# Kernel optimization log

Hardware: AMD Instinct MI355X
Metric: run time of the kernel (lower is better)

Reference implementation:

```python
import jax, jax.numpy as jnp
import numpy as np

N, D, H, G = 4096, 256, 4, 16
HEAD_DIM = D // H
LN_EPS = 1e-5
TEMP = 5.0


def setup_inputs() -> dict:
    key = jax.random.key(0)
    ks = jax.random.split(key, 12)
    s = 0.05  # weight init scale
    nrm = lambda k, shp: jax.random.normal(k, shp, jnp.float32) * s
    return {
        "x": jax.random.normal(ks[0], (N, D), jnp.float32),
        "Wq": nrm(ks[1], (D, D)), "bq": jnp.zeros((D,), jnp.float32),
        "Wk": nrm(ks[2], (D, D)), "bk": jnp.zeros((D,), jnp.float32),
        "Wv": nrm(ks[3], (D, D)), "bv": jnp.zeros((D,), jnp.float32),
        "Wv1": nrm(ks[4], (D, D // 2)), "bv1": jnp.zeros((D // 2,), jnp.float32),
        "Wv2": nrm(ks[5], (D // 2, 1)), "bv2": jnp.zeros((1,), jnp.float32),
        "Wc1": nrm(ks[6], (2 * D, D)), "bc1": jnp.zeros((D,), jnp.float32),
        "Wc2": nrm(ks[7], (D, 1)), "bc2": jnp.zeros((1,), jnp.float32),
        "gamma": jnp.ones((D,), jnp.float32),
        "beta": jnp.zeros((D,), jnp.float32),
        "batch": jnp.sort(jax.random.randint(ks[8], (N,), 0, G)),
    }


def reference(x, Wq, bq, Wk, bk, Wv, bv, Wv1, bv1, Wv2, bv2,
              Wc1, bc1, Wc2, bc2, gamma, beta, batch):
    n = x.shape[0]
    # multi-head projections -> [N, H, head_dim]
    Q = (x @ Wq + bq).reshape(n, H, HEAD_DIM)
    K = (x @ Wk + bk).reshape(n, H, HEAD_DIM)
    V = (x @ Wv + bv).reshape(n, H, HEAD_DIM)

    # dense scores [N, N, H], block-diagonal mask by graph membership
    scores = jnp.einsum('nhd,mhd->nmh', Q, K) / np.sqrt(HEAD_DIM).astype(np.float32)
    same_graph = (batch[:, None] == batch[None, :])  # [N, N]
    scores = jnp.where(same_graph[:, :, None], scores, -jnp.inf)
    probs = jax.nn.softmax(scores, axis=1)  # softmax over keys m (dim=1, as in torch)
    # dropout is identity in eval mode
    attended = jnp.einsum('nmh,mhd->nhd', probs, V).reshape(n, D)

    # vulnerability detector MLP: D -> D/2 -> 1, sigmoid
    vuln = jax.nn.sigmoid(jax.nn.relu(x @ Wv1 + bv1) @ Wv2 + bv2)[:, 0]

    # global max pool per graph, broadcast back to nodes
    graph_ctx = jax.ops.segment_max(x, batch, num_segments=G, indices_are_sorted=True)[batch]
    combined = jnp.concatenate([x, graph_ctx], axis=1)  # [N, 2D]
    ctx = jax.nn.sigmoid(jnp.tanh(combined @ Wc1 + bc1) @ Wc2 + bc2)[:, 0]

    mha_avg = probs.mean(axis=(1, 2))  # [N]
    w = 0.6 * vuln + 0.3 * ctx + 0.1 * mha_avg

    # per-graph segment softmax with temperature 5.0
    w5 = w * TEMP
    seg_max = jax.ops.segment_max(w5, batch, num_segments=G, indices_are_sorted=True)[batch]
    e = jnp.exp(w5 - seg_max)
    seg_sum = jax.ops.segment_sum(e, batch, num_segments=G, indices_are_sorted=True)[batch]
    att = e / seg_sum  # [N]

    out = attended * att[:, None] + x  # residual
    # LayerNorm over last dim
    mu = out.mean(axis=-1, keepdims=True)
    var = out.var(axis=-1, keepdims=True)
    out = (out - mu) * jax.lax.rsqrt(var + LN_EPS) * gamma + beta
    return out, att
```

## Files before the change

### kernel.cpp

```cpp
#include <hip/hip_runtime.h>
#include <math.h>

#define N_NODES 4096
#define DIM 256
#define NH 4
#define NG 16
#define LN_EPS 1e-5f
#define TEMP 5.0f
#define RSLACK 4160
#define PS_STRIDE 72
#define BS_STRIDE 264
#define QT_MAX 24
#define KC3 3
#define ATTN_BLOCKS (NG * QT_MAX * KC3)

typedef __attribute__((ext_vector_type(8))) short short8;
typedef __attribute__((ext_vector_type(4))) short short4_t;
typedef __attribute__((ext_vector_type(4))) float f32x4;

__device__ __forceinline__ unsigned short f2bf(float f) {
    unsigned u = __builtin_bit_cast(unsigned, f);
    u += 0x7FFFu + ((u >> 16) & 1u);
    return (unsigned short)(u >> 16);
}
__device__ __forceinline__ float bf2f(unsigned short u) {
    return __builtin_bit_cast(float, (unsigned)u << 16);
}
__device__ __forceinline__ float fsigmoid(float z) { return 1.f / (1.f + __expf(-z)); }
__device__ __forceinline__ float ftanh(float z) {
    float t = __expf(2.f * z);
    return (t - 1.f) / (t + 1.f);
}
__device__ __forceinline__ int seg_search(const int* __restrict__ batch, int g) {
    int lo = 0, hi = N_NODES;
    while (lo < hi) {
        int mid = (lo + hi) >> 1;
        if (batch[mid] < g) lo = mid + 1; else hi = mid;
    }
    return lo;
}

__device__ __forceinline__ short8 afrag_f32(const float* __restrict__ x, int row, int k0) {
    float4 a = *(const float4*)&x[(size_t)row * 256 + k0];
    float4 b = *(const float4*)&x[(size_t)row * 256 + k0 + 4];
    short8 r = {(short)f2bf(a.x), (short)f2bf(a.y), (short)f2bf(a.z), (short)f2bf(a.w),
                (short)f2bf(b.x), (short)f2bf(b.y), (short)f2bf(b.z), (short)f2bf(b.w)};
    return r;
}

__device__ __forceinline__ void ldsB(const float* __restrict__ W, int ws, int bn,
                                     unsigned short* __restrict__ Bs) {
    int c4 = (threadIdx.x & 15) * 4;
    int r0 = threadIdx.x >> 4;
    for (int p = 0; p < 16; ++p) {
        int k = p * 16 + r0;
        float4 wv = *(const float4*)&W[(size_t)k * ws + bn + c4];
        Bs[(c4 + 0) * BS_STRIDE + k] = f2bf(wv.x);
        Bs[(c4 + 1) * BS_STRIDE + k] = f2bf(wv.y);
        Bs[(c4 + 2) * BS_STRIDE + k] = f2bf(wv.z);
        Bs[(c4 + 3) * BS_STRIDE + k] = f2bf(wv.w);
    }
    __syncthreads();
}

__global__ __launch_bounds__(256) void k1_kernel(
    const float* __restrict__ x,
    const float* __restrict__ Wq, const float* __restrict__ bq,
    const float* __restrict__ Wk, const float* __restrict__ bk,
    const float* __restrict__ Wv, const float* __restrict__ bv,
    const float* __restrict__ Wv1, const float* __restrict__ bv1,
    const float* __restrict__ Wv2, const float* __restrict__ Wc1,
    const float* __restrict__ bc1, const int* __restrict__ batch,
    unsigned short* __restrict__ Qb, unsigned short* __restrict__ Kb,
    unsigned short* __restrict__ Vt, float* __restrict__ vacc2,
    float* __restrict__ Tpre, float* __restrict__ gcw, int* __restrict__ seg) {
    __shared__ __align__(16) char smem[64 * BS_STRIDE * 2];
    int id = blockIdx.x, tid = threadIdx.x;
    if (id < 16) {
        int g = id;
        int s = seg_search(batch, g), e = seg_search(batch, g + 1);
        float* red = (float*)smem;
        float* gl  = (float*)smem + 1024;
        int c4 = (tid & 63) * 4, way = tid >> 6;
        float4 mx = {-INFINITY, -INFINITY, -INFINITY, -INFINITY};
        for (int i = s + way; i < e; i += 4) {
            float4 v = *(const float4*)&x[(size_t)i * DIM + c4];
            mx.x = fmaxf(mx.x, v.x); mx.y = fmaxf(mx.y, v.y);
            mx.z = fmaxf(mx.z, v.z); mx.w = fmaxf(mx.w, v.w);
        }
        *(float4*)&red[way * 256 + c4] = mx;
        __syncthreads();
        if (way == 0) {
#pragma unroll
            for (int j = 0; j < 4; ++j) {
                float mm = fmaxf(fmaxf(red[c4 + j], red[256 + c4 + j]),
                                 fmaxf(red[512 + c4 + j], red[768 + c4 + j]));
                gl[c4 + j] = bf2f(f2bf(mm));
            }
        }
        __syncthreads();
        float a0 = 0.f, a1 = 0.f, a2 = 0.f, a3 = 0.f;
        for (int k = 0; k < 256; k += 4) {
            a0 += gl[k + 0] * Wc1[(size_t)(256 + k + 0) * 256 + tid];
            a1 += gl[k + 1] * Wc1[(size_t)(256 + k + 1) * 256 + tid];
            a2 += gl[k + 2] * Wc1[(size_t)(256 + k + 2) * 256 + tid];
            a3 += gl[k + 3] * Wc1[(size_t)(256 + k + 3) * 256 + tid];
        }
        gcw[g * 256 + tid] = (a0 + a1) + (a2 + a3);
        return;
    }
    if (id == 16) {
        if (tid <= NG) seg[tid] = seg_search(batch, tid);
        return;
    }
    int u = id - 17;
    unsigned short* Bs = (unsigned short*)smem;
    int w = tid >> 6, lane = tid & 63, m = lane & 15, quad = lane >> 4;
    if (u < 768) {
        int z = u >> 8, r = u & 255, bx = r & 63, by = r >> 6;
        const float* W = (z == 0) ? Wq : (z == 1) ? Wk : Wv;
        const float* bias = (z == 0) ? bq : (z == 1) ? bk : bv;
        ldsB(W, 256, by * 64, Bs);
        int rowA = bx * 64 + 16 * w + m;
        short8 a[8];
#pragma unroll
        for (int ks = 0; ks < 8; ++ks) a[ks] = afrag_f32(x, rowA, ks * 32 + quad * 8);
        int node0 = bx * 64 + 16 * w + quad * 4;
#pragma unroll
        for (int nt = 0; nt < 4; ++nt) {
            f32x4 acc = {0.f, 0.f, 0.f, 0.f};
#pragma unroll
            for (int ks = 0; ks < 8; ++ks) {
                short8 b = *(const short8*)&Bs[(nt * 16 + m) * BS_STRIDE + ks * 32 + quad * 8];
                acc = __builtin_amdgcn_mfma_f32_16x16x32_bf16(a[ks], b, acc, 0, 0, 0);
            }
            int col = by * 64 + nt * 16 + m;
            float bb = bias[col];
            if (z == 0) {
#pragma unroll
                for (int r2 = 0; r2 < 4; ++r2)
                    Qb[(size_t)(node0 + r2) * 256 + col] = f2bf((acc[r2] + bb) * 0.125f);
            } else if (z == 1) {
#pragma unroll
                for (int r2 = 0; r2 < 4; ++r2)
                    Kb[(size_t)(node0 + r2) * 256 + col] = f2bf(acc[r2] + bb);
            } else {
                short4_t pk = {(short)f2bf(acc[0] + bb), (short)f2bf(acc[1] + bb),
                               (short)f2bf(acc[2] + bb), (short)f2bf(acc[3] + bb)};
                *(short4_t*)&Vt[(size_t)col * RSLACK + node0] = pk;
            }
        }
    } else if (u < 896) {
        int r = u - 768, bx = r & 63, by = r >> 6;
        ldsB(Wv1, 128, by * 64, Bs);
        int rowA = bx * 64 + 16 * w + m;
        short8 a[8];
#pragma unroll
        for (int ks = 0; ks < 8; ++ks) a[ks] = afrag_f32(x, rowA, ks * 32 + quad * 8);
        int node0 = bx * 64 + 16 * w + quad * 4;
        float psum[4] = {0.f, 0.f, 0.f, 0.f};
#pragma unroll
        for (int nt = 0; nt < 4; ++nt) {
            f32x4 acc = {0.f, 0.f, 0.f, 0.f};
#pragma unroll
            for (int ks = 0; ks < 8; ++ks) {
                short8 b = *(const short8*)&Bs[(nt * 16 + m) * BS_STRIDE + ks * 32 + quad * 8];
                acc = __builtin_amdgcn_mfma_f32_16x16x32_bf16(a[ks], b, acc, 0, 0, 0);
            }
            int col = by * 64 + nt * 16 + m;
            float bb = bv1[col], wv = Wv2[col];
#pragma unroll
            for (int r2 = 0; r2 < 4; ++r2) psum[r2] += fmaxf(acc[r2] + bb, 0.f) * wv;
        }
#pragma unroll
        for (int r2 = 0; r2 < 4; ++r2) {
#pragma unroll
            for (int mm = 1; mm < 16; mm <<= 1) psum[r2] += __shfl_xor(psum[r2], mm);
            if (m == 0) vacc2[(size_t)(node0 + r2) * 2 + by] = psum[r2];
        }
    } else {
        int r = u - 896, bx = r & 63, by = r >> 6;
        ldsB(Wc1, 256, by * 64, Bs);
        int rowA = bx * 64 + 16 * w + m;
        short8 a[8];
#pragma unroll
        for (int ks = 0; ks < 8; ++ks) a[ks] = afrag_f32(x, rowA, ks * 32 + quad * 8);
        int node0 = bx * 64 + 16 * w + quad * 4;
#pragma unroll
        for (int nt = 0; nt < 4; ++nt) {
            f32x4 acc = {0.f, 0.f, 0.f, 0.f};
#pragma unroll
            for (int ks = 0; ks < 8; ++ks) {
                short8 b = *(const short8*)&Bs[(nt * 16 + m) * BS_STRIDE + ks * 32 + quad * 8];
                acc = __builtin_amdgcn_mfma_f32_16x16x32_bf16(a[ks], b, acc, 0, 0, 0);
            }
            int col = by * 64 + nt * 16 + m;
            float bb = bc1[col];
#pragma unroll
            for (int r2 = 0; r2 < 4; ++r2)
                Tpre[(size_t)(node0 + r2) * 256 + col] = acc[r2] + bb;
        }
    }
}

__global__ __launch_bounds__(256) void k2_kernel(
    const float* __restrict__ Tpre, const float* __restrict__ gcw,
    const float* __restrict__ Wc2, const int* __restrict__ batch,
    const unsigned short* __restrict__ Qb, const unsigned short* __restrict__ Kb,
    const unsigned short* __restrict__ Vt, const int* __restrict__ seg,
    unsigned short* __restrict__ Opart, float* __restrict__ Lpart,
    float* __restrict__ cacc) {
    __shared__ __align__(16) unsigned short Ps[4 * 16 * PS_STRIDE];
    int tid = threadIdx.x;
    if (blockIdx.x < 256) {
        int nl = tid >> 4, cs = (tid & 15) * 16;
        int node = blockIdx.x * 16 + nl;
        int g = batch[node];
        float sum = 0.f;
#pragma unroll
        for (int j = 0; j < 16; ++j) {
            int c = cs + j;
            sum += ftanh(Tpre[(size_t)node * 256 + c] + gcw[g * 256 + c]) * Wc2[c];
        }
#pragma unroll
        for (int mm = 1; mm < 16; mm <<= 1) sum += __shfl_xor(sum, mm);
        if ((tid & 15) == 0) cacc[node] = sum;
        return;
    }
    int w = tid >> 6, lane = tid & 63, m = lane & 15, quad = lane >> 4;
    int wid = (blockIdx.x - 256) * 4 + w;
    int g = wid / (KC3 * QT_MAX * NH);
    int r1 = wid - g * (KC3 * QT_MAX * NH);
    int kc = r1 / (QT_MAX * NH);
    int r2i = r1 - kc * (QT_MAX * NH);
    int qt = r2i >> 2, h = r2i & 3;
    int s = seg[g], e = seg[g + 1];
    int q0 = s + qt * 16;
    int kst = s + kc * 128;
    if (q0 >= e || kst >= e) return;
    int ken = min(e, kst + 128);

    short8 qa0 = *(const short8*)&Qb[(size_t)(q0 + m) * 256 + h * 64 + quad * 8];
    short8 qa1 = *(const short8*)&Qb[(size_t)(q0 + m) * 256 + h * 64 + 32 + quad * 8];
    short8 ones = {16256, 16256, 16256, 16256, 16256, 16256, 16256, 16256};
    f32x4 O[4];
    f32x4 Lacc = {0.f, 0.f, 0.f, 0.f};
#pragma unroll
    for (int nt = 0; nt < 4; ++nt) O[nt] = (f32x4){0.f, 0.f, 0.f, 0.f};
    int wbase = w * 16 * PS_STRIDE;

    for (int k0 = kst; k0 < ken; k0 += 64) {
        f32x4 S[4];
#pragma unroll
        for (int nt = 0; nt < 4; ++nt) {
            int key = k0 + nt * 16 + m;
            short8 kb0 = *(const short8*)&Kb[(size_t)key * 256 + h * 64 + quad * 8];
            short8 kb1 = *(const short8*)&Kb[(size_t)key * 256 + h * 64 + 32 + quad * 8];
            f32x4 sa = {0.f, 0.f, 0.f, 0.f};
            sa = __builtin_amdgcn_mfma_f32_16x16x32_bf16(qa0, kb0, sa, 0, 0, 0);
            sa = __builtin_amdgcn_mfma_f32_16x16x32_bf16(qa1, kb1, sa, 0, 0, 0);
            S[nt] = sa;
        }
        __builtin_amdgcn_wave_barrier();
#pragma unroll
        for (int nt = 0; nt < 4; ++nt) {
            bool valid = (k0 + nt * 16 + m) < e;
#pragma unroll
            for (int r3 = 0; r3 < 4; ++r3) {
                float p = valid ? __expf(S[nt][r3]) : 0.f;
                Ps[wbase + (quad * 4 + r3) * PS_STRIDE + nt * 16 + m] = f2bf(p);
            }
        }
        __builtin_amdgcn_wave_barrier();
        short8 pa0 = *(const short8*)&Ps[wbase + m * PS_STRIDE + quad * 8];
        short8 pa1 = *(const short8*)&Ps[wbase + m * PS_STRIDE + 32 + quad * 8];
        Lacc = __builtin_amdgcn_mfma_f32_16x16x32_bf16(pa0, ones, Lacc, 0, 0, 0);
        Lacc = __builtin_amdgcn_mfma_f32_16x16x32_bf16(pa1, ones, Lacc, 0, 0, 0);
#pragma unroll
        for (int nt = 0; nt < 4; ++nt) {
            const unsigned short* vrow = &Vt[(size_t)(h * 64 + nt * 16 + m) * RSLACK + k0];
            short8 vb0 = *(const short8*)&vrow[quad * 8];
            short8 vb1 = *(const short8*)&vrow[32 + quad * 8];
            O[nt] = __builtin_amdgcn_mfma_f32_16x16x32_bf16(pa0, vb0, O[nt], 0, 0, 0);
            O[nt] = __builtin_amdgcn_mfma_f32_16x16x32_bf16(pa1, vb1, O[nt], 0, 0, 0);
        }
    }
#pragma unroll
    for (int r3 = 0; r3 < 4; ++r3) {
        int q = q0 + quad * 4 + r3;
        if (q < e) {
            if (m == 0) Lpart[((size_t)kc * N_NODES + q) * 4 + h] = Lacc[r3];
#pragma unroll
            for (int nt = 0; nt < 4; ++nt)
                Opart[((size_t)kc * N_NODES + q) * 256 + h * 64 + nt * 16 + m] =
                    f2bf(O[nt][r3]);
        }
    }
}

__global__ __launch_bounds__(256) void k3_kernel(
    const unsigned short* __restrict__ Opart, const float* __restrict__ Lpart,
    const float* __restrict__ x, const float* __restrict__ vacc2,
    const float* __restrict__ cacc, const float* __restrict__ bv2,
    const float* __restrict__ bc2, const float* __restrict__ gamma,
    const float* __restrict__ beta, const int* __restrict__ batch,
    const int* __restrict__ seg, float* __restrict__ out,
    float* __restrict__ att_out) {
    __shared__ float wsc[776];
    __shared__ float gm[8], gsum[8];
    __shared__ float r1[4], r2[4];
    int tid = threadIdx.x;
    int n0 = blockIdx.x * 8;
    int gf = batch[n0], gl = batch[n0 + 7];
    int s0 = seg[gf], e1 = seg[gl + 1];
    float vb = bv2[0], cb = bc2[0];
    for (int j = s0 + tid; j < e1; j += 256) {
        float2 vv = *(const float2*)&vacc2[(size_t)j * 2];
        wsc[j - s0] = TEMP * (0.6f * fsigmoid(vv.x + vv.y + vb) +
                              0.3f * fsigmoid(cacc[j] + cb) + 0.1f / 4096.f);
    }
    __syncthreads();
    for (int g = gf; g <= gl; ++g) {
        int gs_ = seg[g], ge = seg[g + 1];
        float mx = -1e30f;
        for (int j = gs_ + tid; j < ge; j += 256) mx = fmaxf(mx, wsc[j - s0]);
#pragma unroll
        for (int k2 = 32; k2; k2 >>= 1) mx = fmaxf(mx, __shfl_xor(mx, k2));
        if ((tid & 63) == 0) r1[tid >> 6] = mx;
        __syncthreads();
        mx = fmaxf(fmaxf(r1[0], r1[1]), fmaxf(r1[2], r1[3]));
        float sm = 0.f;
        for (int j = gs_ + tid; j < ge; j += 256) sm += __expf(wsc[j - s0] - mx);
#pragma unroll
        for (int k2 = 32; k2; k2 >>= 1) sm += __shfl_xor(sm, k2);
        __syncthreads();
        if ((tid & 63) == 0) r2[tid >> 6] = sm;
        __syncthreads();
        if (tid == 0) {
            gm[g - gf] = mx;
            gsum[g - gf] = r2[0] + r2[1] + r2[2] + r2[3];
        }
        __syncthreads();
    }
    int h = tid >> 6;
    for (int i = 0; i < 8; ++i) {
        int n = n0 + i;
        int g = batch[n];
        int s = seg[g], e = seg[g + 1];
        float att_n = __expf(wsc[n - s0] - gm[g - gf]) / gsum[g - gf];
        if (tid == 0) att_out[n] = att_n;
        float L = 0.f, O = 0.f;
#pragma unroll
        for (int c = 0; c < KC3; ++c) {
            bool valid = (s + c * 128) < e;
            float lv = Lpart[((size_t)c * N_NODES + n) * 4 + h];
            float ov = bf2f(Opart[((size_t)c * N_NODES + n) * 256 + tid]);
            if (valid) { L += lv; O += ov; }
        }
        float o = (O / L) * att_n + x[(size_t)n * 256 + tid];
        float s1 = o, s2 = o * o;
#pragma unroll
        for (int k2 = 32; k2; k2 >>= 1) {
            s1 += __shfl_xor(s1, k2);
            s2 += __shfl_xor(s2, k2);
        }
        __syncthreads();
        if ((tid & 63) == 0) { r1[tid >> 6] = s1; r2[tid >> 6] = s2; }
        __syncthreads();
        float mu = (r1[0] + r1[1] + r1[2] + r1[3]) * (1.f / 256.f);
        float ms = (r2[0] + r2[1] + r2[2] + r2[3]) * (1.f / 256.f);
        float rs = rsqrtf(ms - mu * mu + LN_EPS);
        out[(size_t)n * 256 + tid] = (o - mu) * rs * gamma[tid] + beta[tid];
    }
}

extern "C" void kernel_launch(void* const* d_in, const int* in_sizes, int n_in,
                              void* d_out, int out_size, void* d_ws, size_t ws_size,
                              hipStream_t stream) {
    const float* x     = (const float*)d_in[0];
    const float* Wq    = (const float*)d_in[1];
    const float* bq    = (const float*)d_in[2];
    const float* Wk    = (const float*)d_in[3];
    const float* bk    = (const float*)d_in[4];
    const float* Wv    = (const float*)d_in[5];
    const float* bv    = (const float*)d_in[6];
    const float* Wv1   = (const float*)d_in[7];
    const float* bv1   = (const float*)d_in[8];
    const float* Wv2   = (const float*)d_in[9];
    const float* bv2   = (const float*)d_in[10];
    const float* Wc1   = (const float*)d_in[11];
    const float* bc1   = (const float*)d_in[12];
    const float* Wc2   = (const float*)d_in[13];
    const float* bc2   = (const float*)d_in[14];
    const float* gamma = (const float*)d_in[15];
    const float* beta  = (const float*)d_in[16];
    const int*   batch = (const int*)d_in[17];

    float* out = (float*)d_out;
    float* att = out + N_NODES * DIM;

    float* vacc2 = (float*)d_ws;
    float* cacc  = vacc2 + N_NODES * 2;
    float* gcw   = cacc + N_NODES;
    float* Lpart = gcw + NG * DIM;
    float* Tpre  = Lpart + KC3 * N_NODES * 4;
    int*   seg   = (int*)(Tpre + N_NODES * DIM);
    unsigned short* Qb    = (unsigned short*)(seg + 32);
    unsigned short* Kb    = Qb + RSLACK * DIM;
    unsigned short* Vt    = Kb + RSLACK * DIM;
    unsigned short* Opart = Vt + DIM * RSLACK;

    k1_kernel<<<1169, 256, 0, stream>>>(x, Wq, bq, Wk, bk, Wv, bv, Wv1, bv1, Wv2,
                                        Wc1, bc1, batch, Qb, Kb, Vt, vacc2, Tpre,
                                        gcw, seg);
    k2_kernel<<<256 + ATTN_BLOCKS, 256, 0, stream>>>(Tpre, gcw, Wc2, batch,
                                                     Qb, Kb, Vt, seg,
                                                     Opart, Lpart, cacc);
    k3_kernel<<<N_NODES / 8, 256, 0, stream>>>(Opart, Lpart, x, vacc2, cacc,
                                               bv2, bc2, gamma, beta, batch, seg,
                                               out, att);
}
```

Before: 166.4 us.

## Halve GEMM tile width and remap blocks by XCD for L2 locality

The projection GEMM tiles shrink from 64 to 32 output columns, doubling the k1 block count to 2304 and halving LDS per block. The vuln partial sums grow from two to four slots per node to match. Block indices in k1 and the attention part of k2 are remapped so blocks sharing the same x rows, or the same graph and key chunk, are spread round-robin over the 8 XCDs, aiming for better L2 reuse. In k2 each wave now handles one head within a block instead of a flat wave index. The cost is that each x row fragment is converted from fp32 and loaded twice as often, with more blocks to schedule.

```diff
diff --git a/kernel.cpp b/kernel.cpp
--- a/kernel.cpp
+++ b/kernel.cpp
@@ -12,7 +12,7 @@
 #define BS_STRIDE 264
 #define QT_MAX 24
 #define KC3 3
-#define ATTN_BLOCKS (NG * QT_MAX * KC3)
+#define ATTN_BLOCKS (NG * KC3 * QT_MAX)
 
 typedef __attribute__((ext_vector_type(8))) short short8;
 typedef __attribute__((ext_vector_type(4))) short short4_t;
@@ -48,12 +48,12 @@
     return r;
 }
 
-__device__ __forceinline__ void ldsB(const float* __restrict__ W, int ws, int bn,
-                                     unsigned short* __restrict__ Bs) {
-    int c4 = (threadIdx.x & 15) * 4;
-    int r0 = threadIdx.x >> 4;
-    for (int p = 0; p < 16; ++p) {
-        int k = p * 16 + r0;
+__device__ __forceinline__ void ldsB32(const float* __restrict__ W, int ws, int bn,
+                                       unsigned short* __restrict__ Bs) {
+    int c4 = (threadIdx.x & 7) * 4;
+    int r0 = threadIdx.x >> 3;
+    for (int p = 0; p < 8; ++p) {
+        int k = p * 32 + r0;
         float4 wv = *(const float4*)&W[(size_t)k * ws + bn + c4];
         Bs[(c4 + 0) * BS_STRIDE + k] = f2bf(wv.x);
         Bs[(c4 + 1) * BS_STRIDE + k] = f2bf(wv.y);
@@ -72,9 +72,9 @@
     const float* __restrict__ Wv2, const float* __restrict__ Wc1,
     const float* __restrict__ bc1, const int* __restrict__ batch,
     unsigned short* __restrict__ Qb, unsigned short* __restrict__ Kb,
-    unsigned short* __restrict__ Vt, float* __restrict__ vacc2,
+    unsigned short* __restrict__ Vt, float* __restrict__ vacc4,
     float* __restrict__ Tpre, float* __restrict__ gcw, int* __restrict__ seg) {
-    __shared__ __align__(16) char smem[64 * BS_STRIDE * 2];
+    __shared__ __align__(16) char smem[32 * BS_STRIDE * 2];
     int id = blockIdx.x, tid = threadIdx.x;
     if (id < 16) {
         int g = id;
@@ -113,28 +113,31 @@
         if (tid <= NG) seg[tid] = seg_search(batch, tid);
         return;
     }
-    int u = id - 17;
+    int p = id - 17;
+    int xcd = p & 7, j = p >> 3;
+    int bx = xcd * 8 + j / 36;
+    int t = j % 36;
     unsigned short* Bs = (unsigned short*)smem;
     int w = tid >> 6, lane = tid & 63, m = lane & 15, quad = lane >> 4;
-    if (u < 768) {
-        int z = u >> 8, r = u & 255, bx = r & 63, by = r >> 6;
+    int rowA = bx * 64 + 16 * w + m;
+    int node0 = bx * 64 + 16 * w + quad * 4;
+    if (t < 24) {
+        int z = t >> 3, by = t & 7;
         const float* W = (z == 0) ? Wq : (z == 1) ? Wk : Wv;
         const float* bias = (z == 0) ? bq : (z == 1) ? bk : bv;
-        ldsB(W, 256, by * 64, Bs);
-        int rowA = bx * 64 + 16 * w + m;
+        ldsB32(W, 256, by * 32, Bs);
         short8 a[8];
 #pragma unroll
         for (int ks = 0; ks < 8; ++ks) a[ks] = afrag_f32(x, rowA, ks * 32 + quad * 8);
-        int node0 = bx * 64 + 16 * w + quad * 4;
-#pragma unroll
-        for (int nt = 0; nt < 4; ++nt) {
+#pragma unroll
+        for (int nt = 0; nt < 2; ++nt) {
             f32x4 acc = {0.f, 0.f, 0.f, 0.f};
 #pragma unroll
             for (int ks = 0; ks < 8; ++ks) {
                 short8 b = *(const short8*)&Bs[(nt * 16 + m) * BS_STRIDE + ks * 32 + quad * 8];
                 acc = __builtin_amdgcn_mfma_f32_16x16x32_bf16(a[ks], b, acc, 0, 0, 0);
             }
-            int col = by * 64 + nt * 16 + m;
+            int col = by * 32 + nt * 16 + m;
             float bb = bias[col];
             if (z == 0) {
 #pragma unroll
@@ -150,24 +153,22 @@
                 *(short4_t*)&Vt[(size_t)col * RSLACK + node0] = pk;
             }
         }
-    } else if (u < 896) {
-        int r = u - 768, bx = r & 63, by = r >> 6;
-        ldsB(Wv1, 128, by * 64, Bs);
-        int rowA = bx * 64 + 16 * w + m;
+    } else if (t < 28) {
+        int by = t - 24;
+        ldsB32(Wv1, 128, by * 32, Bs);
         short8 a[8];
 #pragma unroll
         for (int ks = 0; ks < 8; ++ks) a[ks] = afrag_f32(x, rowA, ks * 32 + quad * 8);
-        int node0 = bx * 64 + 16 * w + quad * 4;
         float psum[4] = {0.f, 0.f, 0.f, 0.f};
 #pragma unroll
-        for (int nt = 0; nt < 4; ++nt) {
+        for (int nt = 0; nt < 2; ++nt) {
             f32x4 acc = {0.f, 0.f, 0.f, 0.f};
 #pragma unroll
             for (int ks = 0; ks < 8; ++ks) {
                 short8 b = *(const short8*)&Bs[(nt * 16 + m) * BS_STRIDE + ks * 32 + quad * 8];
                 acc = __builtin_amdgcn_mfma_f32_16x16x32_bf16(a[ks], b, acc, 0, 0, 0);
             }
-            int col = by * 64 + nt * 16 + m;
+            int col = by * 32 + nt * 16 + m;
             float bb = bv1[col], wv = Wv2[col];
 #pragma unroll
             for (int r2 = 0; r2 < 4; ++r2) psum[r2] += fmaxf(acc[r2] + bb, 0.f) * wv;
@@ -176,25 +177,23 @@
         for (int r2 = 0; r2 < 4; ++r2) {
 #pragma unroll
             for (int mm = 1; mm < 16; mm <<= 1) psum[r2] += __shfl_xor(psum[r2], mm);
-            if (m == 0) vacc2[(size_t)(node0 + r2) * 2 + by] = psum[r2];
+            if (m == 0) vacc4[(size_t)(node0 + r2) * 4 + by] = psum[r2];
         }
     } else {
-        int r = u - 896, bx = r & 63, by = r >> 6;
-        ldsB(Wc1, 256, by * 64, Bs);
-        int rowA = bx * 64 + 16 * w + m;
+        int by = t - 28;
+        ldsB32(Wc1, 256, by * 32, Bs);
         short8 a[8];
 #pragma unroll
         for (int ks = 0; ks < 8; ++ks) a[ks] = afrag_f32(x, rowA, ks * 32 + quad * 8);
-        int node0 = bx * 64 + 16 * w + quad * 4;
-#pragma unroll
-        for (int nt = 0; nt < 4; ++nt) {
+#pragma unroll
+        for (int nt = 0; nt < 2; ++nt) {
             f32x4 acc = {0.f, 0.f, 0.f, 0.f};
 #pragma unroll
             for (int ks = 0; ks < 8; ++ks) {
                 short8 b = *(const short8*)&Bs[(nt * 16 + m) * BS_STRIDE + ks * 32 + quad * 8];
                 acc = __builtin_amdgcn_mfma_f32_16x16x32_bf16(a[ks], b, acc, 0, 0, 0);
             }
-            int col = by * 64 + nt * 16 + m;
+            int col = by * 32 + nt * 16 + m;
             float bb = bc1[col];
 #pragma unroll
             for (int r2 = 0; r2 < 4; ++r2)
@@ -218,8 +217,8 @@
         int g = batch[node];
         float sum = 0.f;
 #pragma unroll
-        for (int j = 0; j < 16; ++j) {
-            int c = cs + j;
+        for (int jj = 0; jj < 16; ++jj) {
+            int c = cs + jj;
             sum += ftanh(Tpre[(size_t)node * 256 + c] + gcw[g * 256 + c]) * Wc2[c];
         }
 #pragma unroll
@@ -227,13 +226,13 @@
         if ((tid & 15) == 0) cacc[node] = sum;
         return;
     }
+    int p = blockIdx.x - 256;
+    int xcd = p & 7, j = p >> 3;
+    int gk = xcd * 6 + j / 24;
+    int qt = j % 24;
+    int g = gk / 3, kc = gk - 3 * (gk / 3);
     int w = tid >> 6, lane = tid & 63, m = lane & 15, quad = lane >> 4;
-    int wid = (blockIdx.x - 256) * 4 + w;
-    int g = wid / (KC3 * QT_MAX * NH);
-    int r1 = wid - g * (KC3 * QT_MAX * NH);
-    int kc = r1 / (QT_MAX * NH);
-    int r2i = r1 - kc * (QT_MAX * NH);
-    int qt = r2i >> 2, h = r2i & 3;
+    int h = w;
     int s = seg[g], e = seg[g + 1];
     int q0 = s + qt * 16;
     int kst = s + kc * 128;
@@ -267,8 +266,8 @@
             bool valid = (k0 + nt * 16 + m) < e;
 #pragma unroll
             for (int r3 = 0; r3 < 4; ++r3) {
-                float p = valid ? __expf(S[nt][r3]) : 0.f;
-                Ps[wbase + (quad * 4 + r3) * PS_STRIDE + nt * 16 + m] = f2bf(p);
+                float pp = valid ? __expf(S[nt][r3]) : 0.f;
+                Ps[wbase + (quad * 4 + r3) * PS_STRIDE + nt * 16 + m] = f2bf(pp);
             }
         }
         __builtin_amdgcn_wave_barrier();
@@ -300,7 +299,7 @@
 
 __global__ __launch_bounds__(256) void k3_kernel(
     const unsigned short* __restrict__ Opart, const float* __restrict__ Lpart,
-    const float* __restrict__ x, const float* __restrict__ vacc2,
+    const float* __restrict__ x, const float* __restrict__ vacc4,
     const float* __restrict__ cacc, const float* __restrict__ bv2,
     const float* __restrict__ bc2, const float* __restrict__ gamma,
     const float* __restrict__ beta, const int* __restrict__ batch,
@@ -315,8 +314,9 @@
     int s0 = seg[gf], e1 = seg[gl + 1];
     float vb = bv2[0], cb = bc2[0];
     for (int j = s0 + tid; j < e1; j += 256) {
-        float2 vv = *(const float2*)&vacc2[(size_t)j * 2];
-        wsc[j - s0] = TEMP * (0.6f * fsigmoid(vv.x + vv.y + vb) +
+        float4 vv = *(const float4*)&vacc4[(size_t)j * 4];
+        float vsum = (vv.x + vv.y) + (vv.z + vv.w);
+        wsc[j - s0] = TEMP * (0.6f * fsigmoid(vsum + vb) +
                               0.3f * fsigmoid(cacc[j] + cb) + 0.1f / 4096.f);
     }
     __syncthreads();
@@ -399,8 +399,8 @@
     float* out = (float*)d_out;
     float* att = out + N_NODES * DIM;
 
-    float* vacc2 = (float*)d_ws;
-    float* cacc  = vacc2 + N_NODES * 2;
+    float* vacc4 = (float*)d_ws;
+    float* cacc  = vacc4 + N_NODES * 4;
     float* gcw   = cacc + N_NODES;
     float* Lpart = gcw + NG * DIM;
     float* Tpre  = Lpart + KC3 * N_NODES * 4;
@@ -410,13 +410,13 @@
     unsigned short* Vt    = Kb + RSLACK * DIM;
     unsigned short* Opart = Vt + DIM * RSLACK;
 
-    k1_kernel<<<1169, 256, 0, stream>>>(x, Wq, bq, Wk, bk, Wv, bv, Wv1, bv1, Wv2,
-                                        Wc1, bc1, batch, Qb, Kb, Vt, vacc2, Tpre,
-                                        gcw, seg);
+    k1_kernel<<<17 + 2304, 256, 0, stream>>>(x, Wq, bq, Wk, bk, Wv, bv, Wv1, bv1,
+                                             Wv2, Wc1, bc1, batch, Qb, Kb, Vt,
+                                             vacc4, Tpre, gcw, seg);
     k2_kernel<<<256 + ATTN_BLOCKS, 256, 0, stream>>>(Tpre, gcw, Wc2, batch,
                                                      Qb, Kb, Vt, seg,
                                                      Opart, Lpart, cacc);
-    k3_kernel<<<N_NODES / 8, 256, 0, stream>>>(Opart, Lpart, x, vacc2, cacc,
+    k3_kernel<<<N_NODES / 8, 256, 0, stream>>>(Opart, Lpart, x, vacc4, cacc,
                                                bv2, bc2, gamma, beta, batch, seg,
                                                out, att);
 }
```

Result: slower. 179.5 us (+7.9%).
